# Optimization experiments

Measured on AMD Instinct MI355X. Metric: run time of the kernel, lower is better.

## Reference

```python
import jax, jax.numpy as jnp
import numpy as np

GRID_SIZE = 5
SPLINE_ORDER = 3
GRID_LO, GRID_HI = -1.0, 1.0
N_COEFF = GRID_SIZE + SPLINE_ORDER  # 8


def make_grid(in_features):
    # (in_features, grid_size + 2*spline_order + 1) = (in, 12)
    h = (GRID_HI - GRID_LO) / GRID_SIZE
    g = jnp.arange(-SPLINE_ORDER, GRID_SIZE + SPLINE_ORDER + 1, dtype=jnp.float32) * h + GRID_LO
    return jnp.broadcast_to(g, (in_features, g.shape[0]))


def b_splines(x, grid):
    # x: (N, in); grid: (in, G). Returns (N, in, grid_size+spline_order).
    xe = x[..., None]
    bases = ((xe >= grid[:, :-1]) & (xe < grid[:, 1:])).astype(x.dtype)
    for k in range(1, SPLINE_ORDER + 1):
        left = (xe - grid[:, :-(k + 1)]) / (grid[:, k:-1] - grid[:, :-(k + 1)]) * bases[..., :-1]
        right = (grid[:, k + 1:] - xe) / (grid[:, k + 1:] - grid[:, 1:-k]) * bases[..., 1:]
        bases = left + right
    return bases


def kan_linear(x, base_w, spline_w, scaler, grid):
    # base branch: SiLU(x) @ base_w^T
    base_out = jax.nn.silu(x) @ base_w.T
    # spline branch: basis (N,in,c) contracted with scaled spline weight (out,in,c)
    b = b_splines(x, grid)
    sw = spline_w * scaler[..., None]
    spline_out = jnp.einsum('nic,oic->no', b, sw)
    return base_out + spline_out


def setup_inputs() -> dict:
    key = jax.random.key(0)
    ks = jax.random.split(key, 7)
    d_model, d_hid = 512, 2049  # d_ff + 1
    s = 0.1  # keep activations roughly inside grid range
    return {
        "x": jax.random.normal(ks[0], (4096, d_model), dtype=jnp.float32) * 0.3,
        "base_w1": jax.random.normal(ks[1], (d_hid, d_model), dtype=jnp.float32) * s,
        "spline_w1": jax.random.normal(ks[2], (d_hid, d_model, N_COEFF), dtype=jnp.float32) * s,
        "scaler1": jax.random.normal(ks[3], (d_hid, d_model), dtype=jnp.float32) * s,
        "base_w2": jax.random.normal(ks[4], (d_model, d_hid), dtype=jnp.float32) * s,
        "spline_w2": jax.random.normal(ks[5], (d_model, d_hid, N_COEFF), dtype=jnp.float32) * s,
        "scaler2": jax.random.normal(ks[6], (d_model, d_hid), dtype=jnp.float32) * s,
    }


def reference(x, base_w1, spline_w1, scaler1, base_w2, spline_w2, scaler2):
    grid1 = make_grid(x.shape[-1])
    h = kan_linear(x, base_w1, spline_w1, scaler1, grid1)
    grid2 = make_grid(h.shape[-1])
    out = kan_linear(h, base_w2, spline_w2, scaler2, grid2)
    return out
```

## Files before the change

### kernel.cpp

```cpp
#include <hip/hip_runtime.h>
#include <hip/hip_bf16.h>

#define T_TOK 4096
#define I1    512
#define O1    2049
#define O1P   2176
#define K1    4608
#define NG1   576
#define I2    2049
#define O2    512
#define K2    18560
#define NG2   2320
#define HLD   2176
#define SPLITS2 8
#define KLEN2 2368
#define NBY   32

typedef __attribute__((ext_vector_type(8))) short short8;
typedef __attribute__((ext_vector_type(4))) float floatx4;
typedef __attribute__((address_space(3))) void* lds_ptr_t;
typedef const __attribute__((address_space(1))) void* gmem_ptr_t;

__device__ __forceinline__ unsigned short f2bf(float f) {
  union { __hip_bfloat16 h; unsigned short u; } cv;
  cv.h = __float2bfloat16(f);
  return cv.u;
}
__device__ __forceinline__ unsigned bfr(float f) {
  union { float f; unsigned u; } c; c.f = f;
  return (c.u + 0x8000u) >> 16;
}
__device__ __forceinline__ float silu_f(float x) { return x / (1.0f + __expf(-x)); }

__device__ __forceinline__ uint4 spline_pack(float h) {
  float u = (h + 2.2f) * 2.5f;
  int ji = (int)u;
  ji = ji < 0 ? 0 : (ji > 10 ? 10 : ji);
  float t = u - (float)ji;
  float it = 1.0f - t, t2 = t * t, t3 = t2 * t;
  float b0 = it * it * it * (1.0f / 6.0f);
  float b1 = (3.0f * t3 - 6.0f * t2 + 4.0f) * (1.0f / 6.0f);
  float b2 = (-3.0f * t3 + 3.0f * t2 + 3.0f * t + 1.0f) * (1.0f / 6.0f);
  float b3 = t3 * (1.0f / 6.0f);
  unsigned pk01 = bfr(b0) | (bfr(b1) << 16);
  unsigned pk23 = bfr(b2) | (bfr(b3) << 16);
  unsigned long long p64 = (unsigned long long)pk01 | ((unsigned long long)pk23 << 32);
  bool inR = (h >= -2.2f) && (h < 2.2f);
  p64 = inR ? p64 : 0ull;
  int sh = (ji - 3) * 16;
  int shr = sh < 0 ? -sh : 0;
  int shl = sh < 0 ? 0 : sh;
  __uint128_t v = ((__uint128_t)(p64 >> shr)) << shl;
  union { __uint128_t q; uint4 u4; } cv;
  cv.q = v;
  return cv.u4;
}

__global__ void pack_w1_kernel(const float* __restrict__ bw, const float* __restrict__ sw,
                               const float* __restrict__ sc, unsigned short* __restrict__ W) {
  int k = blockIdx.x * 256 + threadIdx.x;
  int o = blockIdx.y;
  float v = 0.0f;
  if (o < O1) {
    if (k < 4096) v = sw[(size_t)o * 4096 + k] * sc[(size_t)o * I1 + (k >> 3)];
    else          v = bw[(size_t)o * I1 + (k - 4096)];
  }
  W[(size_t)o * K1 + k] = f2bf(v);
}

__global__ void pack_w2_kernel(const float* __restrict__ bw, const float* __restrict__ sw,
                               const float* __restrict__ sc, unsigned short* __restrict__ W) {
  int k = blockIdx.x * 256 + threadIdx.x;
  if (k >= K2) return;
  int o = blockIdx.y;
  float v = 0.0f;
  if (k < 16392)      v = sw[(size_t)o * 16392 + k] * sc[(size_t)o * I2 + (k >> 3)];
  else if (k < 18441) v = bw[(size_t)o * I2 + (k - 16392)];
  W[(size_t)o * K2 + k] = f2bf(v);
}

__global__ void expand1_kernel(const float* __restrict__ x, unsigned short* __restrict__ A) {
  int g = blockIdx.x * 256 + threadIdx.x;
  if (g >= NG1) return;
  int m = blockIdx.y;
  uint4 val;
  if (g < 512) {
    val = spline_pack(x[(size_t)m * I1 + g]);
  } else {
    const float4* xr = (const float4*)(x + (size_t)m * I1 + (size_t)(g - 512) * 8);
    float4 a = xr[0], b = xr[1];
    union { unsigned short s[8]; uint4 v; } pk;
    pk.s[0] = f2bf(silu_f(a.x)); pk.s[1] = f2bf(silu_f(a.y));
    pk.s[2] = f2bf(silu_f(a.z)); pk.s[3] = f2bf(silu_f(a.w));
    pk.s[4] = f2bf(silu_f(b.x)); pk.s[5] = f2bf(silu_f(b.y));
    pk.s[6] = f2bf(silu_f(b.z)); pk.s[7] = f2bf(silu_f(b.w));
    val = pk.v;
  }
  *(uint4*)(A + (size_t)m * K1 + (size_t)g * 8) = val;
}

__global__ void expand2_kernel(const float* __restrict__ H, unsigned short* __restrict__ A) {
  int g = blockIdx.x * 256 + threadIdx.x;
  if (g >= NG2) return;
  int m = blockIdx.y;
  uint4 val;
  if (g < 2049) {
    val = spline_pack(H[(size_t)m * HLD + g]);
  } else if (g < 2306) {
    int c0 = (g - 2049) * 8;
    union { unsigned short s[8]; uint4 v; } pk;
#pragma unroll
    for (int c = 0; c < 8; ++c) {
      int idx = c0 + c;
      float v = (idx < I2) ? silu_f(H[(size_t)m * HLD + idx]) : 0.0f;
      pk.s[c] = f2bf(v);
    }
    val = pk.v;
  } else {
    val = make_uint4(0u, 0u, 0u, 0u);
  }
  *(uint4*)(A + (size_t)m * K2 + (size_t)g * 8) = val;
}

__global__ __launch_bounds__(256, 4)
void gemm_bt_kernel(const unsigned short* __restrict__ Aw, const unsigned short* __restrict__ Bw,
                    float* __restrict__ C, int Ktot, int N, int ldc, int kLen,
                    int nBx, int storeMode)
{
  __shared__ __align__(16) unsigned short As[128 * 64];
  __shared__ __align__(16) unsigned short Bs[128 * 64];

  const int Lb = blockIdx.x;
  const int m8 = Lb & 7;
  const int r  = Lb >> 3;
  const int bx = r % nBx;
  const int p  = m8 + ((r / nBx) << 3);
  const int by = p & (NBY - 1);
  const int bz = p >> 5;

  const int tid = threadIdx.x;
  const int ks = bz * kLen;
  int ke = ks + kLen; if (ke > Ktot) ke = Ktot;

  const int w = tid >> 6, L = tid & 63, q = L >> 4, ln = L & 15;
  const int wm = (w & 1) << 6, wn = (w >> 1) << 6;

  floatx4 zf = {0.f, 0.f, 0.f, 0.f};
  floatx4 acc[4][4];
#pragma unroll
  for (int mt = 0; mt < 4; ++mt)
#pragma unroll
    for (int nt = 0; nt < 4; ++nt)
      acc[mt][nt] = zf;

  const unsigned short* ga[4];
  const unsigned short* gb[4];
  int ldsOff[4];
#pragma unroll
  for (int r4 = 0; r4 < 4; ++r4) {
    int e = r4 * 256 + tid;
    int br = e >> 3;
    int cg = (e & 7) ^ (br & 7);
    ga[r4] = Aw + ((long)by * 128 + br) * (long)Ktot + ks + cg * 8;
    gb[r4] = Bw + ((long)bx * 128 + br) * (long)Ktot + ks + cg * 8;
    ldsOff[r4] = e * 8;
  }

  for (int kc = ks; kc < ke; kc += 64) {
    __syncthreads();
#pragma unroll
    for (int r4 = 0; r4 < 4; ++r4) {
      __builtin_amdgcn_global_load_lds((gmem_ptr_t)ga[r4], (lds_ptr_t)&As[ldsOff[r4]], 16, 0, 0);
      ga[r4] += 64;
      __builtin_amdgcn_global_load_lds((gmem_ptr_t)gb[r4], (lds_ptr_t)&Bs[ldsOff[r4]], 16, 0, 0);
      gb[r4] += 64;
    }
    __syncthreads();

#pragma unroll
    for (int s = 0; s < 2; ++s) {
      short8 af[4], bf[4];
#pragma unroll
      for (int mt = 0; mt < 4; ++mt) {
        int rr = wm + mt * 16 + ln;
        int cl = ((s << 2) | q) ^ (rr & 7);
        af[mt] = *(const short8*)&As[rr * 64 + cl * 8];
      }
#pragma unroll
      for (int nt = 0; nt < 4; ++nt) {
        int rr = wn + nt * 16 + ln;
        int cl = ((s << 2) | q) ^ (rr & 7);
        bf[nt] = *(const short8*)&Bs[rr * 64 + cl * 8];
      }
#pragma unroll
      for (int mt = 0; mt < 4; ++mt)
#pragma unroll
        for (int nt = 0; nt < 4; ++nt)
          acc[mt][nt] = __builtin_amdgcn_mfma_f32_16x16x32_bf16(af[mt], bf[nt], acc[mt][nt], 0, 0, 0);
    }
  }

  if (storeMode == 0) {
#pragma unroll
    for (int mt = 0; mt < 4; ++mt) {
#pragma unroll
      for (int nt = 0; nt < 4; ++nt) {
        int n = bx * 128 + wn + nt * 16 + ln;
        if (n < N) {
          int m0 = by * 128 + wm + mt * 16 + q * 4;
#pragma unroll
          for (int rg = 0; rg < 4; ++rg)
            C[(size_t)(m0 + rg) * ldc + n] = acc[mt][nt][rg];
        }
      }
    }
  } else {
#pragma unroll
    for (int mt = 0; mt < 4; ++mt) {
#pragma unroll
      for (int nt = 0; nt < 4; ++nt) {
        int n = bx * 128 + wn + nt * 16 + ln;
        if (n < N) {
          int m0 = by * 128 + wm + mt * 16 + q * 4;
#pragma unroll
          for (int rg = 0; rg < 4; ++rg)
            atomicAdd(&C[(size_t)(m0 + rg) * ldc + n], acc[mt][nt][rg]);
        }
      }
    }
  }
}

extern "C" void kernel_launch(void* const* d_in, const int* in_sizes, int n_in,
                              void* d_out, int out_size, void* d_ws, size_t ws_size,
                              hipStream_t stream) {
  const float* x   = (const float*)d_in[0];
  const float* bw1 = (const float*)d_in[1];
  const float* sw1 = (const float*)d_in[2];
  const float* sc1 = (const float*)d_in[3];
  const float* bw2 = (const float*)d_in[4];
  const float* sw2 = (const float*)d_in[5];
  const float* sc2 = (const float*)d_in[6];
  float* out = (float*)d_out;

  float* H = (float*)d_ws;
  unsigned short* W2 = (unsigned short*)(H + (size_t)T_TOK * HLD);
  unsigned short* A2 = W2 + (size_t)O2 * K2;
  unsigned short* A1 = A2;
  unsigned short* W1 = A1 + (size_t)T_TOK * K1;

  hipMemsetAsync(d_out, 0, (size_t)out_size * sizeof(float), stream);

  pack_w1_kernel<<<dim3(K1 / 256, O1P), 256, 0, stream>>>(bw1, sw1, sc1, W1);
  pack_w2_kernel<<<dim3((K2 + 255) / 256, O2), 256, 0, stream>>>(bw2, sw2, sc2, W2);
  expand1_kernel<<<dim3((NG1 + 255) / 256, T_TOK), 256, 0, stream>>>(x, A1);

  gemm_bt_kernel<<<(O1P / 128) * NBY, 256, 0, stream>>>(
      A1, W1, H, K1, O1, HLD, K1, O1P / 128, 0);

  expand2_kernel<<<dim3((NG2 + 255) / 256, T_TOK), 256, 0, stream>>>(H, A2);

  gemm_bt_kernel<<<(O2 / 128) * NBY * SPLITS2, 256, 0, stream>>>(
      A2, W2, out, K2, O2, O2, KLEN2, O2 / 128, 2);
}
```

Measured before the change: 411.0 us.

## Replace 128x128 GEMM with double-buffered 256x256 tiles and split odd output column

New measurement: 435.3 us. 5.9% more time.

```diff
diff --git a/kernel.cpp b/kernel.cpp
--- a/kernel.cpp
+++ b/kernel.cpp
@@ -4,17 +4,14 @@
 #define T_TOK 4096
 #define I1    512
 #define O1    2049
-#define O1P   2176
 #define K1    4608
 #define NG1   576
 #define I2    2049
 #define O2    512
 #define K2    18560
 #define NG2   2320
-#define HLD   2176
-#define SPLITS2 8
-#define KLEN2 2368
-#define NBY   32
+#define N1G   2048
+#define HPART ((size_t)T_TOK * N1G)
 
 typedef __attribute__((ext_vector_type(8))) short short8;
 typedef __attribute__((ext_vector_type(4))) float floatx4;
@@ -25,6 +22,9 @@
   union { __hip_bfloat16 h; unsigned short u; } cv;
   cv.h = __float2bfloat16(f);
   return cv.u;
+}
+__device__ __forceinline__ float b2f(unsigned short u) {
+  union { float f; unsigned u; } c; c.u = (unsigned)u << 16; return c.f;
 }
 __device__ __forceinline__ unsigned bfr(float f) {
   union { float f; unsigned u; } c; c.f = f;
@@ -60,11 +60,9 @@
                                const float* __restrict__ sc, unsigned short* __restrict__ W) {
   int k = blockIdx.x * 256 + threadIdx.x;
   int o = blockIdx.y;
-  float v = 0.0f;
-  if (o < O1) {
-    if (k < 4096) v = sw[(size_t)o * 4096 + k] * sc[(size_t)o * I1 + (k >> 3)];
-    else          v = bw[(size_t)o * I1 + (k - 4096)];
-  }
+  float v;
+  if (k < 4096) v = sw[(size_t)o * 4096 + k] * sc[(size_t)o * I1 + (k >> 3)];
+  else          v = bw[(size_t)o * I1 + (k - 4096)];
   W[(size_t)o * K1 + k] = f2bf(v);
 }
 
@@ -99,20 +97,49 @@
   *(uint4*)(A + (size_t)m * K1 + (size_t)g * 8) = val;
 }
 
-__global__ void expand2_kernel(const float* __restrict__ H, unsigned short* __restrict__ A) {
+__global__ void gemv_col_kernel(const unsigned short* __restrict__ A1,
+                                const unsigned short* __restrict__ W1,
+                                float* __restrict__ Hcol) {
+  int m = blockIdx.x * 4 + (threadIdx.x >> 6);
+  int lane = threadIdx.x & 63;
+  const unsigned short* a  = A1 + (size_t)m * K1;
+  const unsigned short* wr = W1 + (size_t)2048 * K1;
+  float s = 0.0f;
+#pragma unroll
+  for (int c = 0; c < 9; ++c) {
+    int off = (c * 64 + lane) * 8;
+    short8 av = *(const short8*)(a + off);
+    short8 wv = *(const short8*)(wr + off);
+#pragma unroll
+    for (int j = 0; j < 8; ++j)
+      s += b2f((unsigned short)av[j]) * b2f((unsigned short)wv[j]);
+  }
+#pragma unroll
+  for (int d = 32; d >= 1; d >>= 1) s += __shfl_down(s, d);
+  if (lane == 0) Hcol[m] = s;
+}
+
+__global__ void expand2_kernel(const float* __restrict__ Ha, const float* __restrict__ Hb,
+                               const float* __restrict__ Hcol, unsigned short* __restrict__ A) {
   int g = blockIdx.x * 256 + threadIdx.x;
   if (g >= NG2) return;
   int m = blockIdx.y;
+  float hc = Hcol[m];
   uint4 val;
   if (g < 2049) {
-    val = spline_pack(H[(size_t)m * HLD + g]);
+    float h = (g < N1G) ? Ha[(size_t)m * N1G + g] + Hb[(size_t)m * N1G + g] : hc;
+    val = spline_pack(h);
   } else if (g < 2306) {
     int c0 = (g - 2049) * 8;
     union { unsigned short s[8]; uint4 v; } pk;
 #pragma unroll
     for (int c = 0; c < 8; ++c) {
       int idx = c0 + c;
-      float v = (idx < I2) ? silu_f(H[(size_t)m * HLD + idx]) : 0.0f;
+      float v = 0.0f;
+      if (idx < I2) {
+        float h = (idx < N1G) ? Ha[(size_t)m * N1G + idx] + Hb[(size_t)m * N1G + idx] : hc;
+        v = silu_f(h);
+      }
       pk.s[c] = f2bf(v);
     }
     val = pk.v;
@@ -122,112 +149,179 @@
   *(uint4*)(A + (size_t)m * K2 + (size_t)g * 8) = val;
 }
 
-__global__ __launch_bounds__(256, 4)
-void gemm_bt_kernel(const unsigned short* __restrict__ Aw, const unsigned short* __restrict__ Bw,
-                    float* __restrict__ C, int Ktot, int N, int ldc, int kLen,
-                    int nBx, int storeMode)
+__device__ __forceinline__ void BARv() { asm volatile("s_barrier" ::: "memory"); }
+__device__ __forceinline__ void LGKM0() {
+  asm volatile("s_waitcnt lgkmcnt(0)" ::: "memory");
+  __builtin_amdgcn_sched_barrier(0);
+}
+__device__ __forceinline__ void VM0() { asm volatile("s_waitcnt vmcnt(0)" ::: "memory"); }
+
+__device__ __forceinline__ void read_af(short8* af, const unsigned short* Asp,
+                                        int wmh, int mh, int kk, int q, int ln) {
+#pragma unroll
+  for (int j = 0; j < 4; ++j) {
+    int rr = wmh * 128 + (mh * 4 + j) * 16 + ln;
+    int cl = (kk * 4 + q) ^ (rr & 7);
+    af[j] = *(const short8*)&Asp[rr * 64 + cl * 8];
+  }
+}
+__device__ __forceinline__ void read_bf(short8* bf, const unsigned short* Bsp,
+                                        int wnq, int kk, int q, int ln) {
+#pragma unroll
+  for (int n = 0; n < 4; ++n) {
+    int rb = wnq * 64 + n * 16 + ln;
+    int cl = (kk * 4 + q) ^ (rb & 7);
+    bf[n] = *(const short8*)&Bsp[rb * 64 + cl * 8];
+  }
+}
+
+__global__ __launch_bounds__(512, 2)
+void gemm256_kernel(const unsigned short* __restrict__ Aw, const unsigned short* __restrict__ Bw,
+                    float* __restrict__ C, int Ktot, int kStep, int nBx, int nBz,
+                    int ldc, size_t pslice, int storeMode)
 {
-  __shared__ __align__(16) unsigned short As[128 * 64];
-  __shared__ __align__(16) unsigned short Bs[128 * 64];
+  __shared__ __align__(16) unsigned short As[2][256 * 64];
+  __shared__ __align__(16) unsigned short Bs[2][256 * 64];
 
   const int Lb = blockIdx.x;
-  const int m8 = Lb & 7;
-  const int r  = Lb >> 3;
-  const int bx = r % nBx;
-  const int p  = m8 + ((r / nBx) << 3);
-  const int by = p & (NBY - 1);
-  const int bz = p >> 5;
+  const int wgid = (Lb & 7) * 32 + (Lb >> 3);
+  const int bx = wgid % nBx;
+  const int tq = wgid / nBx;
+  const int by = tq & 15;
+  const int bz = tq >> 4;
 
   const int tid = threadIdx.x;
-  const int ks = bz * kLen;
-  int ke = ks + kLen; if (ke > Ktot) ke = Ktot;
+  const int ks = bz * kStep;
+  const int ke = (bz == nBz - 1) ? Ktot : ks + kStep;
+  const int ntiles = (ke - ks) >> 6;
 
   const int w = tid >> 6, L = tid & 63, q = L >> 4, ln = L & 15;
-  const int wm = (w & 1) << 6, wn = (w >> 1) << 6;
+  const int wmh = w & 1;
+  const int wnq = w >> 1;
 
   floatx4 zf = {0.f, 0.f, 0.f, 0.f};
-  floatx4 acc[4][4];
-#pragma unroll
-  for (int mt = 0; mt < 4; ++mt)
-#pragma unroll
-    for (int nt = 0; nt < 4; ++nt)
-      acc[mt][nt] = zf;
-
-  const unsigned short* ga[4];
-  const unsigned short* gb[4];
-  int ldsOff[4];
-#pragma unroll
-  for (int r4 = 0; r4 < 4; ++r4) {
-    int e = r4 * 256 + tid;
+  floatx4 acc[8][4];
+#pragma unroll
+  for (int f = 0; f < 8; ++f)
+#pragma unroll
+    for (int n = 0; n < 4; ++n)
+      acc[f][n] = zf;
+
+  const unsigned short* gA[4];
+  const unsigned short* gB[4];
+  int ldsO[4];
+#pragma unroll
+  for (int l = 0; l < 4; ++l) {
+    int e = l * 512 + tid;
     int br = e >> 3;
     int cg = (e & 7) ^ (br & 7);
-    ga[r4] = Aw + ((long)by * 128 + br) * (long)Ktot + ks + cg * 8;
-    gb[r4] = Bw + ((long)bx * 128 + br) * (long)Ktot + ks + cg * 8;
-    ldsOff[r4] = e * 8;
-  }
-
-  for (int kc = ks; kc < ke; kc += 64) {
-    __syncthreads();
-#pragma unroll
-    for (int r4 = 0; r4 < 4; ++r4) {
-      __builtin_amdgcn_global_load_lds((gmem_ptr_t)ga[r4], (lds_ptr_t)&As[ldsOff[r4]], 16, 0, 0);
-      ga[r4] += 64;
-      __builtin_amdgcn_global_load_lds((gmem_ptr_t)gb[r4], (lds_ptr_t)&Bs[ldsOff[r4]], 16, 0, 0);
-      gb[r4] += 64;
+    gA[l] = Aw + ((size_t)(by * 256 + br)) * Ktot + ks + cg * 8;
+    gB[l] = Bw + ((size_t)(bx * 256 + br)) * Ktot + ks + cg * 8;
+    ldsO[l] = e * 8;
+  }
+
+  {
+    unsigned short* Asn = (unsigned short*)As[0];
+    unsigned short* Bsn = (unsigned short*)Bs[0];
+#pragma unroll
+    for (int l = 0; l < 4; ++l) {
+      __builtin_amdgcn_global_load_lds((gmem_ptr_t)gA[l], (lds_ptr_t)&Asn[ldsO[l]], 16, 0, 0);
+      gA[l] += 64;
+      __builtin_amdgcn_global_load_lds((gmem_ptr_t)gB[l], (lds_ptr_t)&Bsn[ldsO[l]], 16, 0, 0);
+      gB[l] += 64;
     }
-    __syncthreads();
-
-#pragma unroll
-    for (int s = 0; s < 2; ++s) {
-      short8 af[4], bf[4];
-#pragma unroll
-      for (int mt = 0; mt < 4; ++mt) {
-        int rr = wm + mt * 16 + ln;
-        int cl = ((s << 2) | q) ^ (rr & 7);
-        af[mt] = *(const short8*)&As[rr * 64 + cl * 8];
-      }
-#pragma unroll
-      for (int nt = 0; nt < 4; ++nt) {
-        int rr = wn + nt * 16 + ln;
-        int cl = ((s << 2) | q) ^ (rr & 7);
-        bf[nt] = *(const short8*)&Bs[rr * 64 + cl * 8];
-      }
-#pragma unroll
-      for (int mt = 0; mt < 4; ++mt)
-#pragma unroll
-        for (int nt = 0; nt < 4; ++nt)
-          acc[mt][nt] = __builtin_amdgcn_mfma_f32_16x16x32_bf16(af[mt], bf[nt], acc[mt][nt], 0, 0, 0);
-    }
-  }
-
-  if (storeMode == 0) {
-#pragma unroll
-    for (int mt = 0; mt < 4; ++mt) {
-#pragma unroll
-      for (int nt = 0; nt < 4; ++nt) {
-        int n = bx * 128 + wn + nt * 16 + ln;
-        if (n < N) {
-          int m0 = by * 128 + wm + mt * 16 + q * 4;
-#pragma unroll
-          for (int rg = 0; rg < 4; ++rg)
-            C[(size_t)(m0 + rg) * ldc + n] = acc[mt][nt][rg];
-        }
+  }
+  VM0(); BARv();
+
+  for (int t = 0; t < ntiles; ++t) {
+    unsigned short* Asp = (unsigned short*)As[t & 1];
+    unsigned short* Bsp = (unsigned short*)Bs[t & 1];
+    unsigned short* Asn = (unsigned short*)As[(t & 1) ^ 1];
+    unsigned short* Bsn = (unsigned short*)Bs[(t & 1) ^ 1];
+    const bool pf = (t + 1 < ntiles);
+    short8 af[4], bf[4];
+
+    read_bf(bf, Bsp, wnq, 0, q, ln);
+    read_af(af, Asp, wmh, 0, 0, q, ln);
+    if (pf) {
+#pragma unroll
+      for (int l = 0; l < 4; ++l) {
+        __builtin_amdgcn_global_load_lds((gmem_ptr_t)gA[l], (lds_ptr_t)&Asn[ldsO[l]], 16, 0, 0);
+        gA[l] += 64;
       }
     }
-  } else {
-#pragma unroll
-    for (int mt = 0; mt < 4; ++mt) {
-#pragma unroll
-      for (int nt = 0; nt < 4; ++nt) {
-        int n = bx * 128 + wn + nt * 16 + ln;
-        if (n < N) {
-          int m0 = by * 128 + wm + mt * 16 + q * 4;
-#pragma unroll
-          for (int rg = 0; rg < 4; ++rg)
-            atomicAdd(&C[(size_t)(m0 + rg) * ldc + n], acc[mt][nt][rg]);
-        }
+    BARv(); LGKM0();
+    __builtin_amdgcn_s_setprio(1);
+#pragma unroll
+    for (int j = 0; j < 4; ++j)
+#pragma unroll
+      for (int n = 0; n < 4; ++n)
+        acc[j][n] = __builtin_amdgcn_mfma_f32_16x16x32_bf16(af[j], bf[n], acc[j][n], 0, 0, 0);
+    __builtin_amdgcn_s_setprio(0);
+    BARv();
+
+    read_af(af, Asp, wmh, 1, 0, q, ln);
+    if (pf) {
+#pragma unroll
+      for (int l = 0; l < 4; ++l) {
+        __builtin_amdgcn_global_load_lds((gmem_ptr_t)gB[l], (lds_ptr_t)&Bsn[ldsO[l]], 16, 0, 0);
+        gB[l] += 64;
       }
     }
+    BARv(); LGKM0();
+    __builtin_amdgcn_s_setprio(1);
+#pragma unroll
+    for (int j = 0; j < 4; ++j)
+#pragma unroll
+      for (int n = 0; n < 4; ++n)
+        acc[4 + j][n] = __builtin_amdgcn_mfma_f32_16x16x32_bf16(af[j], bf[n], acc[4 + j][n], 0, 0, 0);
+    __builtin_amdgcn_s_setprio(0);
+    BARv();
+
+    read_bf(bf, Bsp, wnq, 1, q, ln);
+    read_af(af, Asp, wmh, 0, 1, q, ln);
+    BARv(); LGKM0();
+    __builtin_amdgcn_s_setprio(1);
+#pragma unroll
+    for (int j = 0; j < 4; ++j)
+#pragma unroll
+      for (int n = 0; n < 4; ++n)
+        acc[j][n] = __builtin_amdgcn_mfma_f32_16x16x32_bf16(af[j], bf[n], acc[j][n], 0, 0, 0);
+    __builtin_amdgcn_s_setprio(0);
+    BARv();
+
+    read_af(af, Asp, wmh, 1, 1, q, ln);
+    BARv(); LGKM0();
+    __builtin_amdgcn_s_setprio(1);
+#pragma unroll
+    for (int j = 0; j < 4; ++j)
+#pragma unroll
+      for (int n = 0; n < 4; ++n)
+        acc[4 + j][n] = __builtin_amdgcn_mfma_f32_16x16x32_bf16(af[j], bf[n], acc[4 + j][n], 0, 0, 0);
+    __builtin_amdgcn_s_setprio(0);
+    VM0();
+    BARv();
+  }
+
+  const int gmb = by * 256 + wmh * 128 + q * 4;
+  const int gnb = bx * 256 + wnq * 64 + ln;
+  if (storeMode == 0) {
+    float* Cp = C + (size_t)bz * pslice;
+#pragma unroll
+    for (int f = 0; f < 8; ++f)
+#pragma unroll
+      for (int n = 0; n < 4; ++n)
+#pragma unroll
+        for (int rg = 0; rg < 4; ++rg)
+          Cp[(size_t)(gmb + f * 16 + rg) * ldc + (gnb + n * 16)] = acc[f][n][rg];
+  } else {
+#pragma unroll
+    for (int f = 0; f < 8; ++f)
+#pragma unroll
+      for (int n = 0; n < 4; ++n)
+#pragma unroll
+        for (int rg = 0; rg < 4; ++rg)
+          atomicAdd(&C[(size_t)(gmb + f * 16 + rg) * ldc + (gnb + n * 16)], acc[f][n][rg]);
   }
 }
 
@@ -243,23 +337,25 @@
   const float* sc2 = (const float*)d_in[6];
   float* out = (float*)d_out;
 
-  float* H = (float*)d_ws;
-  unsigned short* W2 = (unsigned short*)(H + (size_t)T_TOK * HLD);
+  float* Ha = (float*)d_ws;
+  float* Hb = Ha + HPART;
+  float* Hcol = Hb + HPART;
+  unsigned short* W2 = (unsigned short*)(Hcol + 16384);
   unsigned short* A2 = W2 + (size_t)O2 * K2;
   unsigned short* A1 = A2;
   unsigned short* W1 = A1 + (size_t)T_TOK * K1;
 
   hipMemsetAsync(d_out, 0, (size_t)out_size * sizeof(float), stream);
 
-  pack_w1_kernel<<<dim3(K1 / 256, O1P), 256, 0, stream>>>(bw1, sw1, sc1, W1);
+  pack_w1_kernel<<<dim3(K1 / 256, O1), 256, 0, stream>>>(bw1, sw1, sc1, W1);
   pack_w2_kernel<<<dim3((K2 + 255) / 256, O2), 256, 0, stream>>>(bw2, sw2, sc2, W2);
   expand1_kernel<<<dim3((NG1 + 255) / 256, T_TOK), 256, 0, stream>>>(x, A1);
 
-  gemm_bt_kernel<<<(O1P / 128) * NBY, 256, 0, stream>>>(
-      A1, W1, H, K1, O1, HLD, K1, O1P / 128, 0);
-
-  expand2_kernel<<<dim3((NG2 + 255) / 256, T_TOK), 256, 0, stream>>>(H, A2);
-
-  gemm_bt_kernel<<<(O2 / 128) * NBY * SPLITS2, 256, 0, stream>>>(
-      A2, W2, out, K2, O2, O2, KLEN2, O2 / 128, 2);
-}
+  gemv_col_kernel<<<T_TOK / 4, 256, 0, stream>>>(A1, W1, Hcol);
+
+  gemm256_kernel<<<256, 512, 0, stream>>>(A1, W1, Ha, K1, 2304, 8, 2, N1G, HPART, 0);
+
+  expand2_kernel<<<dim3((NG2 + 255) / 256, T_TOK), 256, 0, stream>>>(Ha, Hb, Hcol, A2);
+
+  gemm256_kernel<<<256, 512, 0, stream>>>(A2, W2, out, K2, 2304, 2, 8, O2, 0, 2);
+}
```

## Split first GEMM over K into two partial buffers and peel odd column into GEMV

Applied to the files above, without the earlier changes.

Measured after the change: 427.8 us. +4.1%, slower.

```diff
diff --git a/kernel.cpp b/kernel.cpp
--- a/kernel.cpp
+++ b/kernel.cpp
@@ -4,16 +4,17 @@
 #define T_TOK 4096
 #define I1    512
 #define O1    2049
-#define O1P   2176
 #define K1    4608
 #define NG1   576
 #define I2    2049
 #define O2    512
 #define K2    18560
 #define NG2   2320
-#define HLD   2176
+#define N1G   2048
+#define HPART ((size_t)T_TOK * N1G)
 #define SPLITS2 8
 #define KLEN2 2368
+#define KLEN1 2304
 #define NBY   32
 
 typedef __attribute__((ext_vector_type(8))) short short8;
@@ -25,6 +26,9 @@
   union { __hip_bfloat16 h; unsigned short u; } cv;
   cv.h = __float2bfloat16(f);
   return cv.u;
+}
+__device__ __forceinline__ float b2f(unsigned short u) {
+  union { float f; unsigned u; } c; c.u = (unsigned)u << 16; return c.f;
 }
 __device__ __forceinline__ unsigned bfr(float f) {
   union { float f; unsigned u; } c; c.f = f;
@@ -60,11 +64,9 @@
                                const float* __restrict__ sc, unsigned short* __restrict__ W) {
   int k = blockIdx.x * 256 + threadIdx.x;
   int o = blockIdx.y;
-  float v = 0.0f;
-  if (o < O1) {
-    if (k < 4096) v = sw[(size_t)o * 4096 + k] * sc[(size_t)o * I1 + (k >> 3)];
-    else          v = bw[(size_t)o * I1 + (k - 4096)];
-  }
+  float v;
+  if (k < 4096) v = sw[(size_t)o * 4096 + k] * sc[(size_t)o * I1 + (k >> 3)];
+  else          v = bw[(size_t)o * I1 + (k - 4096)];
   W[(size_t)o * K1 + k] = f2bf(v);
 }
 
@@ -99,20 +101,49 @@
   *(uint4*)(A + (size_t)m * K1 + (size_t)g * 8) = val;
 }
 
-__global__ void expand2_kernel(const float* __restrict__ H, unsigned short* __restrict__ A) {
+__global__ void gemv_col_kernel(const unsigned short* __restrict__ A1,
+                                const unsigned short* __restrict__ W1,
+                                float* __restrict__ Hcol) {
+  int m = blockIdx.x * 4 + (threadIdx.x >> 6);
+  int lane = threadIdx.x & 63;
+  const unsigned short* a  = A1 + (size_t)m * K1;
+  const unsigned short* wr = W1 + (size_t)2048 * K1;
+  float s = 0.0f;
+#pragma unroll
+  for (int c = 0; c < 9; ++c) {
+    int off = (c * 64 + lane) * 8;
+    short8 av = *(const short8*)(a + off);
+    short8 wv = *(const short8*)(wr + off);
+#pragma unroll
+    for (int j = 0; j < 8; ++j)
+      s += b2f((unsigned short)av[j]) * b2f((unsigned short)wv[j]);
+  }
+#pragma unroll
+  for (int d = 32; d >= 1; d >>= 1) s += __shfl_down(s, d);
+  if (lane == 0) Hcol[m] = s;
+}
+
+__global__ void expand2_kernel(const float* __restrict__ Ha, const float* __restrict__ Hb,
+                               const float* __restrict__ Hcol, unsigned short* __restrict__ A) {
   int g = blockIdx.x * 256 + threadIdx.x;
   if (g >= NG2) return;
   int m = blockIdx.y;
+  float hc = Hcol[m];
   uint4 val;
   if (g < 2049) {
-    val = spline_pack(H[(size_t)m * HLD + g]);
+    float h = (g < N1G) ? Ha[(size_t)m * N1G + g] + Hb[(size_t)m * N1G + g] : hc;
+    val = spline_pack(h);
   } else if (g < 2306) {
     int c0 = (g - 2049) * 8;
     union { unsigned short s[8]; uint4 v; } pk;
 #pragma unroll
     for (int c = 0; c < 8; ++c) {
       int idx = c0 + c;
-      float v = (idx < I2) ? silu_f(H[(size_t)m * HLD + idx]) : 0.0f;
+      float v = 0.0f;
+      if (idx < I2) {
+        float h = (idx < N1G) ? Ha[(size_t)m * N1G + idx] + Hb[(size_t)m * N1G + idx] : hc;
+        v = silu_f(h);
+      }
       pk.s[c] = f2bf(v);
     }
     val = pk.v;
@@ -125,7 +156,7 @@
 __global__ __launch_bounds__(256, 4)
 void gemm_bt_kernel(const unsigned short* __restrict__ Aw, const unsigned short* __restrict__ Bw,
                     float* __restrict__ C, int Ktot, int N, int ldc, int kLen,
-                    int nBx, int storeMode)
+                    int nBx, size_t pslice, int storeMode)
 {
   __shared__ __align__(16) unsigned short As[128 * 64];
   __shared__ __align__(16) unsigned short Bs[128 * 64];
@@ -201,6 +232,7 @@
   }
 
   if (storeMode == 0) {
+    float* Cp = C + (size_t)bz * pslice;
 #pragma unroll
     for (int mt = 0; mt < 4; ++mt) {
 #pragma unroll
@@ -210,7 +242,7 @@
           int m0 = by * 128 + wm + mt * 16 + q * 4;
 #pragma unroll
           for (int rg = 0; rg < 4; ++rg)
-            C[(size_t)(m0 + rg) * ldc + n] = acc[mt][nt][rg];
+            Cp[(size_t)(m0 + rg) * ldc + n] = acc[mt][nt][rg];
         }
       }
     }
@@ -243,23 +275,27 @@
   const float* sc2 = (const float*)d_in[6];
   float* out = (float*)d_out;
 
-  float* H = (float*)d_ws;
-  unsigned short* W2 = (unsigned short*)(H + (size_t)T_TOK * HLD);
+  float* Ha = (float*)d_ws;
+  float* Hb = Ha + HPART;
+  float* Hcol = Hb + HPART;
+  unsigned short* W2 = (unsigned short*)(Hcol + 16384);
   unsigned short* A2 = W2 + (size_t)O2 * K2;
   unsigned short* A1 = A2;
   unsigned short* W1 = A1 + (size_t)T_TOK * K1;
 
   hipMemsetAsync(d_out, 0, (size_t)out_size * sizeof(float), stream);
 
-  pack_w1_kernel<<<dim3(K1 / 256, O1P), 256, 0, stream>>>(bw1, sw1, sc1, W1);
+  pack_w1_kernel<<<dim3(K1 / 256, O1), 256, 0, stream>>>(bw1, sw1, sc1, W1);
   pack_w2_kernel<<<dim3((K2 + 255) / 256, O2), 256, 0, stream>>>(bw2, sw2, sc2, W2);
   expand1_kernel<<<dim3((NG1 + 255) / 256, T_TOK), 256, 0, stream>>>(x, A1);
 
-  gemm_bt_kernel<<<(O1P / 128) * NBY, 256, 0, stream>>>(
-      A1, W1, H, K1, O1, HLD, K1, O1P / 128, 0);
-
-  expand2_kernel<<<dim3((NG2 + 255) / 256, T_TOK), 256, 0, stream>>>(H, A2);
+  gemv_col_kernel<<<T_TOK / 4, 256, 0, stream>>>(A1, W1, Hcol);
+
+  gemm_bt_kernel<<<16 * NBY * 2, 256, 0, stream>>>(
+      A1, W1, Ha, K1, N1G, N1G, KLEN1, 16, HPART, 0);
+
+  expand2_kernel<<<dim3((NG2 + 255) / 256, T_TOK), 256, 0, stream>>>(Ha, Hb, Hcol, A2);
 
   gemm_bt_kernel<<<(O2 / 128) * NBY * SPLITS2, 256, 0, stream>>>(
-      A2, W2, out, K2, O2, O2, KLEN2, O2 / 128, 2);
-}
+      A2, W2, out, K2, O2, O2, KLEN2, 4, 0, 2);
+}
```

## Fuse spline expansion into GEMM1 epilogue and merge prep kernels

Applied to the files above, without the earlier changes.

New measurement: 441.4 us. 1.07x slower.

```diff
diff --git a/kernel.cpp b/kernel.cpp
--- a/kernel.cpp
+++ b/kernel.cpp
@@ -9,12 +9,16 @@
 #define NG1   576
 #define I2    2049
 #define O2    512
-#define K2    18560
-#define NG2   2320
+#define K2P   18496
+#define NG2   2312
 #define HLD   2176
 #define SPLITS2 8
 #define KLEN2 2368
 #define NBY   32
+#define PW1_NB 4896
+#define E1_NB  9216
+#define PW2_NB 8192
+#define E2B_NB 8192
 
 typedef __attribute__((ext_vector_type(8))) short short8;
 typedef __attribute__((ext_vector_type(4))) float floatx4;
@@ -56,76 +60,99 @@
   return cv.u4;
 }
 
-__global__ void pack_w1_kernel(const float* __restrict__ bw, const float* __restrict__ sw,
-                               const float* __restrict__ sc, unsigned short* __restrict__ W) {
-  int k = blockIdx.x * 256 + threadIdx.x;
-  int o = blockIdx.y;
-  float v = 0.0f;
-  if (o < O1) {
-    if (k < 4096) v = sw[(size_t)o * 4096 + k] * sc[(size_t)o * I1 + (k >> 3)];
-    else          v = bw[(size_t)o * I1 + (k - 4096)];
-  }
-  W[(size_t)o * K1 + k] = f2bf(v);
-}
-
-__global__ void pack_w2_kernel(const float* __restrict__ bw, const float* __restrict__ sw,
-                               const float* __restrict__ sc, unsigned short* __restrict__ W) {
-  int k = blockIdx.x * 256 + threadIdx.x;
-  if (k >= K2) return;
-  int o = blockIdx.y;
-  float v = 0.0f;
-  if (k < 16392)      v = sw[(size_t)o * 16392 + k] * sc[(size_t)o * I2 + (k >> 3)];
-  else if (k < 18441) v = bw[(size_t)o * I2 + (k - 16392)];
-  W[(size_t)o * K2 + k] = f2bf(v);
-}
-
-__global__ void expand1_kernel(const float* __restrict__ x, unsigned short* __restrict__ A) {
-  int g = blockIdx.x * 256 + threadIdx.x;
-  if (g >= NG1) return;
-  int m = blockIdx.y;
-  uint4 val;
-  if (g < 512) {
-    val = spline_pack(x[(size_t)m * I1 + g]);
+__global__ void prep1_kernel(const float* __restrict__ x, const float* __restrict__ bw1,
+                             const float* __restrict__ sw1, const float* __restrict__ sc1,
+                             unsigned short* __restrict__ A1, unsigned short* __restrict__ W1) {
+  int b = blockIdx.x;
+  union { unsigned short s[8]; uint4 v; } pk;
+  if (b < PW1_NB) {
+    int idx = b * 256 + threadIdx.x;
+    int o = idx / NG1, g = idx - o * NG1;
+    if (o >= O1) {
+      pk.v = make_uint4(0u, 0u, 0u, 0u);
+    } else if (g < 512) {
+      const float4* p = (const float4*)&sw1[(size_t)o * 4096 + g * 8];
+      float4 a = p[0], c = p[1];
+      float sc = sc1[(size_t)o * I1 + g];
+      pk.s[0] = f2bf(a.x * sc); pk.s[1] = f2bf(a.y * sc);
+      pk.s[2] = f2bf(a.z * sc); pk.s[3] = f2bf(a.w * sc);
+      pk.s[4] = f2bf(c.x * sc); pk.s[5] = f2bf(c.y * sc);
+      pk.s[6] = f2bf(c.z * sc); pk.s[7] = f2bf(c.w * sc);
+    } else {
+      const float4* p = (const float4*)&bw1[(size_t)o * I1 + (g - 512) * 8];
+      float4 a = p[0], c = p[1];
+      pk.s[0] = f2bf(a.x); pk.s[1] = f2bf(a.y); pk.s[2] = f2bf(a.z); pk.s[3] = f2bf(a.w);
+      pk.s[4] = f2bf(c.x); pk.s[5] = f2bf(c.y); pk.s[6] = f2bf(c.z); pk.s[7] = f2bf(c.w);
+    }
+    *(uint4*)&W1[(size_t)o * K1 + (size_t)g * 8] = pk.v;
   } else {
-    const float4* xr = (const float4*)(x + (size_t)m * I1 + (size_t)(g - 512) * 8);
-    float4 a = xr[0], b = xr[1];
-    union { unsigned short s[8]; uint4 v; } pk;
-    pk.s[0] = f2bf(silu_f(a.x)); pk.s[1] = f2bf(silu_f(a.y));
-    pk.s[2] = f2bf(silu_f(a.z)); pk.s[3] = f2bf(silu_f(a.w));
-    pk.s[4] = f2bf(silu_f(b.x)); pk.s[5] = f2bf(silu_f(b.y));
-    pk.s[6] = f2bf(silu_f(b.z)); pk.s[7] = f2bf(silu_f(b.w));
-    val = pk.v;
-  }
-  *(uint4*)(A + (size_t)m * K1 + (size_t)g * 8) = val;
-}
-
-__global__ void expand2_kernel(const float* __restrict__ H, unsigned short* __restrict__ A) {
-  int g = blockIdx.x * 256 + threadIdx.x;
-  if (g >= NG2) return;
-  int m = blockIdx.y;
-  uint4 val;
-  if (g < 2049) {
-    val = spline_pack(H[(size_t)m * HLD + g]);
-  } else if (g < 2306) {
-    int c0 = (g - 2049) * 8;
-    union { unsigned short s[8]; uint4 v; } pk;
-#pragma unroll
-    for (int c = 0; c < 8; ++c) {
-      int idx = c0 + c;
-      float v = (idx < I2) ? silu_f(H[(size_t)m * HLD + idx]) : 0.0f;
-      pk.s[c] = f2bf(v);
-    }
-    val = pk.v;
+    int idx = (b - PW1_NB) * 256 + threadIdx.x;
+    int m = idx / NG1, g = idx - m * NG1;
+    if (g < 512) {
+      pk.v = spline_pack(x[(size_t)m * I1 + g]);
+    } else {
+      const float4* p = (const float4*)&x[(size_t)m * I1 + (size_t)(g - 512) * 8];
+      float4 a = p[0], c = p[1];
+      pk.s[0] = f2bf(silu_f(a.x)); pk.s[1] = f2bf(silu_f(a.y));
+      pk.s[2] = f2bf(silu_f(a.z)); pk.s[3] = f2bf(silu_f(a.w));
+      pk.s[4] = f2bf(silu_f(c.x)); pk.s[5] = f2bf(silu_f(c.y));
+      pk.s[6] = f2bf(silu_f(c.z)); pk.s[7] = f2bf(silu_f(c.w));
+    }
+    *(uint4*)&A1[(size_t)m * K1 + (size_t)g * 8] = pk.v;
+  }
+}
+
+__global__ void mid_kernel(const float* __restrict__ bw2, const float* __restrict__ sw2,
+                           const float* __restrict__ sc2, const float* __restrict__ H,
+                           unsigned short* __restrict__ W2, unsigned short* __restrict__ A2) {
+  int b = blockIdx.x;
+  union { unsigned short s[8]; uint4 v; } pk;
+  if (b < PW2_NB) {
+    int idx = b * 256 + threadIdx.x;
+    int o = idx >> 12, g = idx & 4095;
+    if (g >= NG2) return;
+    if (g < 2049) {
+      const float4* p = (const float4*)&sw2[(size_t)o * 16392 + (size_t)g * 8];
+      float4 a = p[0], c = p[1];
+      float sc = sc2[(size_t)o * I2 + g];
+      pk.s[0] = f2bf(a.x * sc); pk.s[1] = f2bf(a.y * sc);
+      pk.s[2] = f2bf(a.z * sc); pk.s[3] = f2bf(a.w * sc);
+      pk.s[4] = f2bf(c.x * sc); pk.s[5] = f2bf(c.y * sc);
+      pk.s[6] = f2bf(c.z * sc); pk.s[7] = f2bf(c.w * sc);
+    } else if (g < 2306) {
+      int c0 = (g - 2049) * 8;
+#pragma unroll
+      for (int j = 0; j < 8; ++j) {
+        int k = c0 + j;
+        pk.s[j] = (k < I2) ? f2bf(bw2[(size_t)o * I2 + k]) : (unsigned short)0;
+      }
+    } else {
+      pk.v = make_uint4(0u, 0u, 0u, 0u);
+    }
+    *(uint4*)&W2[(size_t)o * K2P + (size_t)g * 8] = pk.v;
   } else {
-    val = make_uint4(0u, 0u, 0u, 0u);
-  }
-  *(uint4*)(A + (size_t)m * K2 + (size_t)g * 8) = val;
+    int idx = (b - PW2_NB) * 256 + threadIdx.x;
+    int m = idx >> 9, g2 = idx & 511;
+    if (g2 >= NG2 - 2049) return;
+    int g = 2049 + g2;
+    if (g < 2306) {
+      int c0 = (g - 2049) * 8;
+#pragma unroll
+      for (int j = 0; j < 8; ++j) {
+        int k = c0 + j;
+        pk.s[j] = (k < I2) ? f2bf(silu_f(H[(size_t)m * HLD + k])) : (unsigned short)0;
+      }
+    } else {
+      pk.v = make_uint4(0u, 0u, 0u, 0u);
+    }
+    *(uint4*)&A2[(size_t)m * K2P + (size_t)g * 8] = pk.v;
+  }
 }
 
 __global__ __launch_bounds__(256, 4)
 void gemm_bt_kernel(const unsigned short* __restrict__ Aw, const unsigned short* __restrict__ Bw,
-                    float* __restrict__ C, int Ktot, int N, int ldc, int kLen,
-                    int nBx, int storeMode)
+                    float* __restrict__ C, unsigned short* __restrict__ A2sp,
+                    int Ktot, int N, int ldc, int kLen, int nBx, int storeMode)
 {
   __shared__ __align__(16) unsigned short As[128 * 64];
   __shared__ __align__(16) unsigned short Bs[128 * 64];
@@ -209,8 +236,11 @@
         if (n < N) {
           int m0 = by * 128 + wm + mt * 16 + q * 4;
 #pragma unroll
-          for (int rg = 0; rg < 4; ++rg)
-            C[(size_t)(m0 + rg) * ldc + n] = acc[mt][nt][rg];
+          for (int rg = 0; rg < 4; ++rg) {
+            float h = acc[mt][nt][rg];
+            C[(size_t)(m0 + rg) * ldc + n] = h;
+            *(uint4*)&A2sp[(size_t)(m0 + rg) * K2P + (size_t)n * 8] = spline_pack(h);
+          }
         }
       }
     }
@@ -244,22 +274,20 @@
   float* out = (float*)d_out;
 
   float* H = (float*)d_ws;
-  unsigned short* W2 = (unsigned short*)(H + (size_t)T_TOK * HLD);
-  unsigned short* A2 = W2 + (size_t)O2 * K2;
-  unsigned short* A1 = A2;
+  unsigned short* A2 = (unsigned short*)(H + (size_t)T_TOK * HLD);
+  unsigned short* A1 = A2 + (size_t)T_TOK * K2P;
   unsigned short* W1 = A1 + (size_t)T_TOK * K1;
+  unsigned short* W2 = A1;
 
   hipMemsetAsync(d_out, 0, (size_t)out_size * sizeof(float), stream);
 
-  pack_w1_kernel<<<dim3(K1 / 256, O1P), 256, 0, stream>>>(bw1, sw1, sc1, W1);
-  pack_w2_kernel<<<dim3((K2 + 255) / 256, O2), 256, 0, stream>>>(bw2, sw2, sc2, W2);
-  expand1_kernel<<<dim3((NG1 + 255) / 256, T_TOK), 256, 0, stream>>>(x, A1);
+  prep1_kernel<<<PW1_NB + E1_NB, 256, 0, stream>>>(x, bw1, sw1, sc1, A1, W1);
 
   gemm_bt_kernel<<<(O1P / 128) * NBY, 256, 0, stream>>>(
-      A1, W1, H, K1, O1, HLD, K1, O1P / 128, 0);
-
-  expand2_kernel<<<dim3((NG2 + 255) / 256, T_TOK), 256, 0, stream>>>(H, A2);
+      A1, W1, H, A2, K1, O1, HLD, K1, O1P / 128, 0);
+
+  mid_kernel<<<PW2_NB + E2B_NB, 256, 0, stream>>>(bw2, sw2, sc2, H, W2, A2);
 
   gemm_bt_kernel<<<(O2 / 128) * NBY * SPLITS2, 256, 0, stream>>>(
-      A2, W2, out, K2, O2, O2, KLEN2, O2 / 128, 2);
-}
+      A2, W2, out, nullptr, K2P, O2, O2, KLEN2, O2 / 128, 2);
+}
```
